# Optimization experiments

Measured on AMD Instinct MI355X. Metric: run time of the kernel, lower is better.

The kernel has to match this reference:

```python
import jax, jax.numpy as jnp
import numpy as np

B, P, NOBJ = 16, 19248, 32
NUM_CLASSES = 81  # 80 foreground + background (code uses num_classes+1 w/o focal loss)
POS_TH, NEG_TH = 0.5, 0.4
VAR0, VAR1 = 0.1, 0.2  # standard SSD encode variances
NEGPOS_RATIO = 3


def setup_inputs() -> dict:
    key = jax.random.key(0)
    k1, k2, k3, k4, k5 = jax.random.split(key, 5)
    loc_data = jax.random.normal(k1, (B, P, 4), jnp.float32)
    conf_data = jax.random.normal(k2, (B, P, NUM_CLASSES), jnp.float32)
    # priors in (cx, cy, w, h), normalized coords
    pc = jax.random.uniform(k3, (P, 2), jnp.float32, 0.05, 0.95)
    pw = jax.random.uniform(jax.random.fold_in(k3, 1), (P, 2), jnp.float32, 0.05, 0.4)
    priors = jnp.concatenate([pc, pw], -1)
    # gt boxes in point form (xmin, ymin, xmax, ymax)
    gc = jax.random.uniform(k4, (B, NOBJ, 2), jnp.float32, 0.2, 0.8)
    gw = jax.random.uniform(jax.random.fold_in(k4, 1), (B, NOBJ, 2), jnp.float32, 0.05, 0.3)
    gt_boxes = jnp.concatenate([gc - gw / 2, gc + gw / 2], -1)
    gt_labels = jax.random.randint(k5, (B, NOBJ), 0, NUM_CLASSES - 1)  # 0..79
    return {"loc_data": loc_data, "conf_data": conf_data, "priors": priors,
            "gt_boxes": gt_boxes, "gt_labels": gt_labels}


def _point_form(p):
    # (cx,cy,w,h) -> (xmin,ymin,xmax,ymax)
    return jnp.concatenate([p[..., :2] - p[..., 2:] / 2, p[..., :2] + p[..., 2:] / 2], -1)


def _jaccard(a, b):
    # a: [N,4], b: [P,4] point form -> IoU [N,P]
    lt = jnp.maximum(a[:, None, :2], b[None, :, :2])
    rb = jnp.minimum(a[:, None, 2:], b[None, :, 2:])
    wh = jnp.clip(rb - lt, 0.0)
    inter = wh[..., 0] * wh[..., 1]
    area_a = (a[:, 2] - a[:, 0]) * (a[:, 3] - a[:, 1])
    area_b = (b[:, 2] - b[:, 0]) * (b[:, 3] - b[:, 1])
    return inter / (area_a[:, None] + area_b[None, :] - inter)


def _match_one(gt, labels, priors_pf, priors):
    # SSD match: per-prior best gt + force each gt's best prior to be positive
    ov = _jaccard(gt, priors_pf)                 # [N,P]
    best_prior_idx = jnp.argmax(ov, axis=1)      # [N]
    best_truth_ov = jnp.max(ov, axis=0)          # [P]
    best_truth_idx = jnp.argmax(ov, axis=0)      # [P]
    best_truth_ov = best_truth_ov.at[best_prior_idx].set(2.0)
    best_truth_idx = best_truth_idx.at[best_prior_idx].set(jnp.arange(gt.shape[0]))
    matched = gt[best_truth_idx]                 # [P,4] point form
    conf = labels[best_truth_idx] + 1
    conf = jnp.where(best_truth_ov < POS_TH, -1, conf)   # neutral band
    conf = jnp.where(best_truth_ov < NEG_TH, 0, conf)    # background
    # encode offsets with variances
    m_cxcy = (matched[:, :2] + matched[:, 2:]) / 2
    m_wh = matched[:, 2:] - matched[:, :2]
    g_cxcy = (m_cxcy - priors[:, :2]) / (VAR0 * priors[:, 2:])
    g_wh = jnp.log(m_wh / priors[:, 2:]) / VAR1
    return jnp.concatenate([g_cxcy, g_wh], -1), conf


def reference(loc_data, conf_data, priors, gt_boxes, gt_labels):
    priors_pf = _point_form(priors)
    loc_t, conf_t = jax.vmap(lambda g, l: _match_one(g, l, priors_pf, priors))(gt_boxes, gt_labels)
    loc_t = jax.lax.stop_gradient(loc_t)
    pos = conf_t > 0                                   # [B,P]
    n_pos = pos.sum(axis=1)                            # [B]
    N = jnp.maximum(pos.sum(), 1).astype(loc_data.dtype)
    # localization: smooth L1 over positives
    d = loc_data - loc_t
    ad = jnp.abs(d)
    sl1 = jnp.where(ad < 1.0, 0.5 * d * d, ad - 0.5)
    loss_l = jnp.sum(sl1 * pos[..., None])
    # confidence: hard negative mining at 3:1
    logp = jax.nn.log_softmax(conf_data, axis=-1)      # [B,P,C]
    ct = jnp.maximum(conf_t, 0)
    nll = -jnp.take_along_axis(logp, ct[..., None], axis=-1)[..., 0]  # [B,P]
    mine = jnp.where(pos | (conf_t < 0), 0.0, nll)     # exclude pos & neutral from mining
    rank = jnp.argsort(jnp.argsort(-mine, axis=1), axis=1)
    num_neg = jnp.minimum(NEGPOS_RATIO * n_pos, P - 1)
    neg = (rank < num_neg[:, None]) & (conf_t == 0)
    loss_c = jnp.sum(nll * (pos | neg))
    return jnp.stack([loss_l, loss_c]) / N
```

## Files before the change

kernel.cpp:

```cpp
#include <hip/hip_runtime.h>
#include <cstdint>
#include <cstddef>

#define BB 16
#define PP 19248
#define NOBJ 32
#define NCLS 81
#define POS_TH 0.5f
#define NEG_TH 0.4f
#define VAR0 0.1f
#define VAR1 0.2f
#define NEGPOS 3

#define MTB 256
#define NMB ((PP + MTB - 1) / MTB)
#define MAINB 1024
#define ROWS_PB 128
#define NSLOT ((PP + ROWS_PB - 1) / ROWS_PB)
#define NSLOTW (NSLOT * 16)
#define ST 1024

#define MCH 8
#define CHLEN (PP / MCH)
#define MJOBS (BB * NOBJ * MCH)
#define MBLK (MJOBS / 4)

#define HSHIFT 19
#define HSIZE 8192
#define HPT (HSIZE / ST)
#define CAP HSIZE

__global__ __launch_bounds__(MTB) void k_match(const float* __restrict__ priors,
                                               const float* __restrict__ gt_boxes,
                                               unsigned long long* __restrict__ gkey) {
    const int wid = threadIdx.x >> 6, lane = threadIdx.x & 63;
    const int job = blockIdx.x * 4 + wid;
    const int b = job >> 8;
    const int n = (job >> 3) & 31;
    const int c = job & 7;

    const float4 g = ((const float4*)gt_boxes)[b * NOBJ + n];
    float garea;
    {
#pragma clang fp contract(off)
        garea = (g.z - g.x) * (g.w - g.y);
    }

    unsigned long long bestkey = 0ull;
    const int pbeg = c * CHLEN;
    const int pend = pbeg + CHLEN;
    for (int p = pbeg + lane; p < pend; p += 64) {
        float4 pr = ((const float4*)priors)[p];
        float iou;
        {
#pragma clang fp contract(off)
            float hw = pr.z / 2.0f, hh = pr.w / 2.0f;
            float px1 = pr.x - hw, py1 = pr.y - hh, px2 = pr.x + hw, py2 = pr.y + hh;
            float parea = (px2 - px1) * (py2 - py1);
            float ix1 = fmaxf(g.x, px1), iy1 = fmaxf(g.y, py1);
            float ix2 = fminf(g.z, px2), iy2 = fminf(g.w, py2);
            float iw = fmaxf(ix2 - ix1, 0.0f), ih = fmaxf(iy2 - iy1, 0.0f);
            float inter = iw * ih;
            iou = inter / (garea + parea - inter);
        }
        unsigned long long key = (((unsigned long long)__float_as_uint(iou)) << 32) |
                                 (unsigned long long)(0xFFFFFFFFu - (unsigned)p);
        if (key > bestkey) bestkey = key;
    }
#pragma unroll
    for (int m = 1; m < 64; m <<= 1) {
        unsigned long long o = __shfl_xor(bestkey, m, 64);
        if (o > bestkey) bestkey = o;
    }
    if (lane == 0) atomicMax(&gkey[b * NOBJ + n], bestkey);
}

__global__ __launch_bounds__(MTB) void k_prior(const float* __restrict__ priors,
                                               const float* __restrict__ gt_boxes,
                                               const int* __restrict__ gt_labels,
                                               unsigned* __restrict__ bp) {
    const int b = blockIdx.y;
    const int p = blockIdx.x * MTB + threadIdx.x;
    __shared__ float4 sg[NOBJ];
    __shared__ int slab[NOBJ];
    if (threadIdx.x < NOBJ) {
        sg[threadIdx.x] = ((const float4*)gt_boxes)[b * NOBJ + threadIdx.x];
        slab[threadIdx.x] = gt_labels[b * NOBJ + threadIdx.x];
    }
    __syncthreads();
    if (p >= PP) return;

    float4 pr = ((const float4*)priors)[p];
    float px1, py1, px2, py2, parea;
    {
#pragma clang fp contract(off)
        float hw = pr.z / 2.0f, hh = pr.w / 2.0f;
        px1 = pr.x - hw; py1 = pr.y - hh; px2 = pr.x + hw; py2 = pr.y + hh;
        parea = (px2 - px1) * (py2 - py1);
    }

    float best = -1.0f;
    int bn = 0;
#pragma unroll 4
    for (int n = 0; n < NOBJ; ++n) {
        float4 g = sg[n];
        float iou;
        {
#pragma clang fp contract(off)
            float ix1 = fmaxf(g.x, px1), iy1 = fmaxf(g.y, py1);
            float ix2 = fminf(g.z, px2), iy2 = fminf(g.w, py2);
            float iw = fmaxf(ix2 - ix1, 0.0f), ih = fmaxf(iy2 - iy1, 0.0f);
            float inter = iw * ih;
            float garea = (g.z - g.x) * (g.w - g.y);
            iou = inter / (garea + parea - inter);
        }
        if (iou > best) { best = iou; bn = n; }
    }
    unsigned cc;
    if (best < NEG_TH) cc = 1u;
    else if (best < POS_TH) cc = 0u;
    else cc = (unsigned)(slab[bn] + 2);
    bp[(size_t)b * PP + p] = ((unsigned)bn << 8) | cc;
}

__global__ __launch_bounds__(512) void k_force(const int* __restrict__ gt_labels,
                                               const unsigned long long* __restrict__ gkey,
                                               unsigned* __restrict__ bp) {
    const int i = threadIdx.x;
    const int b = i >> 5, n = i & 31;
    unsigned long long key = gkey[b * NOBJ + n];
    unsigned pstar = 0xFFFFFFFFu - (unsigned)(key & 0xFFFFFFFFull);
    int lab = gt_labels[b * NOBJ + n];
    unsigned val = 0x80000000u | ((unsigned)n << 8) | (unsigned)(lab + 2);
    atomicMax(&bp[(size_t)b * PP + pstar], val);
}

__device__ __forceinline__ float sl1(float d) {
    float ad = fabsf(d);
    return ad < 1.0f ? 0.5f * d * d : ad - 0.5f;
}

__global__ __launch_bounds__(MAINB) void k_main(const float* __restrict__ loc_data,
                                                const float* __restrict__ conf_data,
                                                const float* __restrict__ priors,
                                                const float* __restrict__ gt_boxes,
                                                const unsigned* __restrict__ bp,
                                                float* __restrict__ mine,
                                                float* __restrict__ p_ll,
                                                float* __restrict__ p_lc,
                                                int* __restrict__ p_np) {
    const int b = blockIdx.y;
    const int t = threadIdx.x;
    const int wid = t >> 6;
    const int lane = t & 63;
    const int g = lane >> 3;
    const int j = lane & 7;
    const int rbase = blockIdx.x * ROWS_PB + wid * 8;
    const int r = rbase + g;
    const bool valid = r < PP;
    const int slot = blockIdx.x * 16 + wid;

    const float* rowp = conf_data + ((size_t)b * PP + r) * NCLS;
    float c[10];
#pragma unroll
    for (int i = 0; i < 10; ++i) c[i] = 0.0f;
    float c80 = 0.0f;
    unsigned w = 1u;
    if (valid) {
#pragma unroll
        for (int i = 0; i < 10; ++i) c[i] = rowp[j + 8 * i];
        if (j == 0) c80 = rowp[80];
        w = bp[(size_t)b * PP + r];
    }

    float s = 0.0f;
#pragma unroll
    for (int i = 0; i < 10; ++i) s += __expf(c[i]);
    if (j == 0) s += __expf(c80);
    s += __shfl_xor(s, 1, 64);
    s += __shfl_xor(s, 2, 64);
    s += __shfl_xor(s, 4, 64);
    const float lse = __logf(s);

    const int cc = (int)(w & 0xFFu);

    float my_ll = 0.0f, my_lc = 0.0f;
    int my_pos = 0;

    if (valid && j == 0) {
        mine[(size_t)b * PP + r] = (cc == 1) ? (lse - c[0]) : 0.0f;
        if (cc >= 2) {
            my_pos = 1;
            my_lc = lse - rowp[cc - 1];
            const int ti = (int)((w >> 8) & 63u);
            float4 gbox = ((const float4*)gt_boxes)[b * NOBJ + ti];
            float4 pr = ((const float4*)priors)[r];
            float mcx = (gbox.x + gbox.z) / 2.0f, mcy = (gbox.y + gbox.w) / 2.0f;
            float mw = gbox.z - gbox.x, mh = gbox.w - gbox.y;
            float t0 = (mcx - pr.x) / (VAR0 * pr.z);
            float t1 = (mcy - pr.y) / (VAR0 * pr.w);
            float t2 = logf(mw / pr.z) / VAR1;
            float t3 = logf(mh / pr.w) / VAR1;
            float4 ld = ((const float4*)loc_data)[(size_t)b * PP + r];
            my_ll = sl1(ld.x - t0) + sl1(ld.y - t1) + sl1(ld.z - t2) + sl1(ld.w - t3);
        }
    }

    if (__ballot(my_pos != 0) == 0ull) {
        if (lane == 0) {
            p_ll[b * NSLOTW + slot] = 0.0f;
            p_lc[b * NSLOTW + slot] = 0.0f;
            p_np[b * NSLOTW + slot] = 0;
        }
    } else {
        for (int off = 32; off > 0; off >>= 1) {
            my_ll += __shfl_down(my_ll, off, 64);
            my_lc += __shfl_down(my_lc, off, 64);
            my_pos += __shfl_down(my_pos, off, 64);
        }
        if (lane == 0) {
            p_ll[b * NSLOTW + slot] = my_ll;
            p_lc[b * NSLOTW + slot] = my_lc;
            p_np[b * NSLOTW + slot] = my_pos;
        }
    }
}

__global__ __launch_bounds__(ST) void k_select(const float* __restrict__ mine,
                                               const float* __restrict__ p_ll,
                                               const float* __restrict__ p_lc,
                                               const int* __restrict__ p_np,
                                               float* __restrict__ acc,
                                               int* __restrict__ acc_np,
                                               unsigned* __restrict__ done,
                                               float* __restrict__ out) {
    const int b = blockIdx.x;
    const int tid = threadIdx.x;
    const int wid = tid >> 6, lane = tid & 63;
    constexpr int NW = ST / 64;

    __shared__ unsigned hist[HSIZE];
    __shared__ unsigned s_tsum[ST];
    __shared__ unsigned s_wsum[NW];
    __shared__ float rll[NW], rlc[NW];
    __shared__ int rnp[NW];
    __shared__ float rs1[NW], rs2[NW];
    __shared__ unsigned rc2[NW];
    __shared__ float s_ll, s_lc, s_neg;
    __shared__ int s_np, s_B, s_G1;
    __shared__ unsigned s_cntB, s_cnt, s_prefix;
    __shared__ int s_rem;
    __shared__ unsigned h16[16];
    __shared__ unsigned swh[NW * 16];
    __shared__ unsigned stot[16];

    float ll = 0.0f, lc = 0.0f;
    int np = 0;
    for (int i = tid; i < NSLOTW; i += ST) {
        ll += p_ll[b * NSLOTW + i];
        lc += p_lc[b * NSLOTW + i];
        np += p_np[b * NSLOTW + i];
    }
    for (int off = 32; off > 0; off >>= 1) {
        ll += __shfl_down(ll, off, 64);
        lc += __shfl_down(lc, off, 64);
        np += __shfl_down(np, off, 64);
    }
    if (lane == 0) { rll[wid] = ll; rlc[wid] = lc; rnp[wid] = np; }
    __syncthreads();
    if (tid == 0) {
        float a = 0.0f, c = 0.0f;
        int n = 0;
        for (int w = 0; w < NW; ++w) { a += rll[w]; c += rlc[w]; n += rnp[w]; }
        s_ll = a; s_lc = c; s_np = n;
        s_neg = 0.0f;
    }
    __syncthreads();
    const int np_b = s_np;
    const int k = min(NEGPOS * np_b, PP - 1);

    const float* mv = mine + (size_t)b * PP;
    const float4* mv4 = (const float4*)mv;
    constexpr int PP4 = PP / 4;

    if (k > 0) {
        for (int i = tid; i < HSIZE; i += ST) hist[i] = 0u;
        __syncthreads();
        for (int i = tid; i < PP4; i += ST) {
            float4 v = mv4[i];
            atomicAdd(&hist[__float_as_uint(v.x) >> HSHIFT], 1u);
            atomicAdd(&hist[__float_as_uint(v.y) >> HSHIFT], 1u);
            atomicAdd(&hist[__float_as_uint(v.z) >> HSHIFT], 1u);
            atomicAdd(&hist[__float_as_uint(v.w) >> HSHIFT], 1u);
        }
        __syncthreads();

        unsigned tsum = 0;
        const int hb = tid * HPT;
#pragma unroll
        for (int v = 0; v < HPT; ++v) tsum += hist[hb + v];
        s_tsum[tid] = tsum;
        unsigned wsum = tsum;
        for (int off = 32; off > 0; off >>= 1) wsum += __shfl_down(wsum, off, 64);
        if (lane == 0) s_wsum[wid] = wsum;
        __syncthreads();
        if (tid == 0) {
            unsigned cum = 0;
            int w = NW - 1;
            for (; w > 0; --w) {
                if (cum + s_wsum[w] >= (unsigned)k) break;
                cum += s_wsum[w];
            }
            int t = (w + 1) * 64 - 1;
            for (; t > w * 64; --t) {
                if (cum + s_tsum[t] >= (unsigned)k) break;
                cum += s_tsum[t];
            }
            int bin = t * HPT + HPT - 1;
            for (; bin > t * HPT; --bin) {
                if (cum + hist[bin] >= (unsigned)k) break;
                cum += hist[bin];
            }
            s_B = bin;
            s_G1 = (int)cum;
            s_cntB = hist[bin];
            s_cnt = 0u;
        }
        __syncthreads();
        const int B = s_B;
        const int r = k - s_G1;
        const unsigned cntB = s_cntB;
        const unsigned bin_lo = (unsigned)B << HSHIFT;
        const unsigned hi_base = (unsigned)(B + 1) << HSHIFT;
        unsigned* cbuf = hist;

        if (cntB <= CAP) {
            float S1 = 0.0f;
            for (int i = tid; i < PP4; i += ST) {
                float4 v = mv4[i];
                unsigned bx = __float_as_uint(v.x);
                unsigned by = __float_as_uint(v.y);
                unsigned bz = __float_as_uint(v.z);
                unsigned bw = __float_as_uint(v.w);
                if (bx >= hi_base) S1 += v.x;
                else if (bx >= bin_lo) cbuf[atomicAdd(&s_cnt, 1u)] = bx;
                if (by >= hi_base) S1 += v.y;
                else if (by >= bin_lo) cbuf[atomicAdd(&s_cnt, 1u)] = by;
                if (bz >= hi_base) S1 += v.z;
                else if (bz >= bin_lo) cbuf[atomicAdd(&s_cnt, 1u)] = bz;
                if (bw >= hi_base) S1 += v.w;
                else if (bw >= bin_lo) cbuf[atomicAdd(&s_cnt, 1u)] = bw;
            }
            for (int off = 32; off > 0; off >>= 1) S1 += __shfl_down(S1, off, 64);
            if (lane == 0) rs1[wid] = S1;
            __syncthreads();

            if (tid == 0) { s_prefix = bin_lo; s_rem = r; }
            __syncthreads();
            for (int pass = 0; pass < 5; ++pass) {
                const int shift = (pass < 4) ? (15 - 4 * pass) : 0;
                const int width = (pass < 4) ? 4 : 3;
                const int nb = 1 << width;
                const unsigned hm = 0xFFFFFFFFu << (shift + width);
                if (tid < 16) h16[tid] = 0u;
                __syncthreads();
                const unsigned prefix = s_prefix;
                for (unsigned i = tid; i < cntB; i += ST) {
                    unsigned bits = cbuf[i];
                    if ((bits & hm) == prefix)
                        atomicAdd(&h16[(bits >> shift) & (nb - 1)], 1u);
                }
                __syncthreads();
                if (tid == 0) {
                    int rem = s_rem;
                    unsigned cum = 0;
                    int chosen = 0;
                    for (int v = nb - 1; v >= 0; --v) {
                        unsigned c = h16[v];
                        if (cum + c >= (unsigned)rem) { chosen = v; s_rem = rem - (int)cum; break; }
                        cum += c;
                    }
                    s_prefix = prefix | ((unsigned)chosen << shift);
                }
                __syncthreads();
            }
            const unsigned T = s_prefix;

            float S2 = 0.0f;
            unsigned c2 = 0;
            for (unsigned i = tid; i < cntB; i += ST) {
                unsigned bits = cbuf[i];
                if (bits > T) { S2 += __uint_as_float(bits); c2++; }
            }
            for (int off = 32; off > 0; off >>= 1) {
                S2 += __shfl_down(S2, off, 64);
                c2 += __shfl_down(c2, off, 64);
            }
            if (lane == 0) { rs2[wid] = S2; rc2[wid] = c2; }
            __syncthreads();
            if (tid == 0) {
                float S1t = 0.0f, S2t = 0.0f;
                unsigned c2t = 0;
                for (int w = 0; w < NW; ++w) { S1t += rs1[w]; S2t += rs2[w]; c2t += rc2[w]; }
                s_neg = S1t + S2t + (float)(r - (int)c2t) * __uint_as_float(T);
            }
            __syncthreads();
        } else {
            if (tid == 0) { s_prefix = 0u; s_rem = k; }
            __syncthreads();
            for (int pass = 0; pass < 8; ++pass) {
                const int shift = 28 - 4 * pass;
                const unsigned hm = (pass == 0) ? 0u : (0xFFFFFFFFu << (shift + 4));
                const unsigned prefix = s_prefix;
                unsigned cnt[16];
#pragma unroll
                for (int v = 0; v < 16; ++v) cnt[v] = 0u;
                for (int i = tid; i < PP; i += ST) {
                    unsigned bits = __float_as_uint(mv[i]);
                    unsigned key = ((bits & hm) == prefix) ? ((bits >> shift) & 15u) : 16u;
                    if (__any(key != 16u)) {
#pragma unroll
                        for (int v = 0; v < 16; ++v)
                            cnt[v] += (unsigned)__popcll(__ballot(key == (unsigned)v));
                    }
                }
                if (lane == 0) {
#pragma unroll
                    for (int v = 0; v < 16; ++v) swh[wid * 16 + v] = cnt[v];
                }
                __syncthreads();
                if (tid < 16) {
                    unsigned tt = 0;
#pragma unroll
                    for (int w = 0; w < NW; ++w) tt += swh[w * 16 + tid];
                    stot[tid] = tt;
                }
                __syncthreads();
                if (tid == 0) {
                    int rem = s_rem;
                    unsigned cum = 0;
                    int chosen = 0;
                    for (int v = 15; v >= 0; --v) {
                        unsigned c = stot[v];
                        if (cum + c >= (unsigned)rem) { chosen = v; s_rem = rem - (int)cum; break; }
                        cum += c;
                    }
                    s_prefix = prefix | ((unsigned)chosen << shift);
                }
                __syncthreads();
            }
            const unsigned T = s_prefix;
            float sum = 0.0f;
            unsigned cnt = 0;
            for (int i = tid; i < PP; i += ST) {
                float v = mv[i];
                if (__float_as_uint(v) > T) { sum += v; cnt++; }
            }
            for (int off = 32; off > 0; off >>= 1) {
                sum += __shfl_down(sum, off, 64);
                cnt += __shfl_down(cnt, off, 64);
            }
            if (lane == 0) { rs2[wid] = sum; rc2[wid] = cnt; }
            __syncthreads();
            if (tid == 0) {
                float S = 0.0f;
                int G = 0;
                for (int w = 0; w < NW; ++w) { S += rs2[w]; G += (int)rc2[w]; }
                s_neg = S + (float)(k - G) * __uint_as_float(T);
            }
            __syncthreads();
        }
    }

    if (tid == 0) {
        atomicAdd(&acc[0], s_ll);
        atomicAdd(&acc[1], s_lc + s_neg);
        atomicAdd(acc_np, np_b);
        __threadfence();
        unsigned prev = atomicAdd(done, 1u);
        if (prev == BB - 1) {
            int tp = atomicAdd(acc_np, 0);
            float N = (float)max(tp, 1);
            float a0 = atomicAdd(&acc[0], 0.0f);
            float a1 = atomicAdd(&acc[1], 0.0f);
            out[0] = a0 / N;
            out[1] = a1 / N;
        }
    }
}

extern "C" void kernel_launch(void* const* d_in, const int* in_sizes, int n_in,
                              void* d_out, int out_size, void* d_ws, size_t ws_size,
                              hipStream_t stream) {
    const float* loc    = (const float*)d_in[0];
    const float* conf   = (const float*)d_in[1];
    const float* priors = (const float*)d_in[2];
    const float* gt     = (const float*)d_in[3];
    const int*   labels = (const int*)d_in[4];
    float* out = (float*)d_out;

    char* ws = (char*)d_ws;
    const size_t SZ_BP = (size_t)BB * PP * 4;
    const size_t SZ_SLOT = (size_t)BB * NSLOTW * 4;
    unsigned long long* gkey = (unsigned long long*)ws;
    float*    acc    = (float*)   (ws + 4096);
    int*      acc_np = (int*)     (ws + 4104);
    unsigned* done   = (unsigned*)(ws + 4108);
    unsigned* bp  = (unsigned*)(ws + 4224);
    float* mine = (float*)(ws + 4224 + SZ_BP);
    float* p_ll = (float*)(ws + 4224 + 2 * SZ_BP);
    float* p_lc = (float*)(ws + 4224 + 2 * SZ_BP + SZ_SLOT);
    int*   p_np = (int*)  (ws + 4224 + 2 * SZ_BP + 2 * SZ_SLOT);

    (void)hipMemsetAsync(ws, 0, 4224, stream);

    k_match<<<MBLK, MTB, 0, stream>>>(priors, gt, gkey);

    dim3 pg(NMB, BB);
    k_prior<<<pg, MTB, 0, stream>>>(priors, gt, labels, bp);

    k_force<<<1, 512, 0, stream>>>(labels, gkey, bp);

    dim3 kg(NSLOT, BB);
    k_main<<<kg, MAINB, 0, stream>>>(loc, conf, priors, gt, bp,
                                     mine, p_ll, p_lc, p_np);

    k_select<<<BB, ST, 0, stream>>>(mine, p_ll, p_lc, p_np, acc, acc_np, done, out);
}
```

Before: 210.7 us.

## Merge match and prior kernels; parallelize bin search and small-bucket select

Combines the per-gt best-prior kernel and the per-prior best-gt kernel into one launch, with block index choosing the role, so one launch and its gap are removed. In the selection kernel, the serial single-thread histogram bin search becomes a wavefront suffix-scan with ballot. When the threshold bucket holds at most 1024 elements, a direct O(n^2) rank-by-comparison replaces the five radix refinement passes and their barriers. The quadratic comparison could cost more when the bucket is near 1024 elements.

```diff
diff --git a/kernel.cpp b/kernel.cpp
--- a/kernel.cpp
+++ b/kernel.cpp
@@ -24,103 +24,105 @@
 #define CHLEN (PP / MCH)
 #define MJOBS (BB * NOBJ * MCH)
 #define MBLK (MJOBS / 4)
+#define MPBLK (MBLK + NMB * BB)
 
 #define HSHIFT 19
 #define HSIZE 8192
 #define HPT (HSIZE / ST)
 #define CAP HSIZE
 
-__global__ __launch_bounds__(MTB) void k_match(const float* __restrict__ priors,
-                                               const float* __restrict__ gt_boxes,
-                                               unsigned long long* __restrict__ gkey) {
-    const int wid = threadIdx.x >> 6, lane = threadIdx.x & 63;
-    const int job = blockIdx.x * 4 + wid;
-    const int b = job >> 8;
-    const int n = (job >> 3) & 31;
-    const int c = job & 7;
-
-    const float4 g = ((const float4*)gt_boxes)[b * NOBJ + n];
-    float garea;
-    {
+__global__ __launch_bounds__(MTB) void k_mp(const float* __restrict__ priors,
+                                            const float* __restrict__ gt_boxes,
+                                            const int* __restrict__ gt_labels,
+                                            unsigned long long* __restrict__ gkey,
+                                            unsigned* __restrict__ bp) {
+    if (blockIdx.x < MBLK) {
+        const int wid = threadIdx.x >> 6, lane = threadIdx.x & 63;
+        const int job = blockIdx.x * 4 + wid;
+        const int b = job >> 8;
+        const int n = (job >> 3) & 31;
+        const int c = job & 7;
+
+        const float4 g = ((const float4*)gt_boxes)[b * NOBJ + n];
+        float garea;
+        {
 #pragma clang fp contract(off)
-        garea = (g.z - g.x) * (g.w - g.y);
-    }
-
-    unsigned long long bestkey = 0ull;
-    const int pbeg = c * CHLEN;
-    const int pend = pbeg + CHLEN;
-    for (int p = pbeg + lane; p < pend; p += 64) {
+            garea = (g.z - g.x) * (g.w - g.y);
+        }
+
+        unsigned long long bestkey = 0ull;
+        const int pbeg = c * CHLEN;
+        const int pend = pbeg + CHLEN;
+        for (int p = pbeg + lane; p < pend; p += 64) {
+            float4 pr = ((const float4*)priors)[p];
+            float iou;
+            {
+#pragma clang fp contract(off)
+                float hw = pr.z / 2.0f, hh = pr.w / 2.0f;
+                float px1 = pr.x - hw, py1 = pr.y - hh, px2 = pr.x + hw, py2 = pr.y + hh;
+                float parea = (px2 - px1) * (py2 - py1);
+                float ix1 = fmaxf(g.x, px1), iy1 = fmaxf(g.y, py1);
+                float ix2 = fminf(g.z, px2), iy2 = fminf(g.w, py2);
+                float iw = fmaxf(ix2 - ix1, 0.0f), ih = fmaxf(iy2 - iy1, 0.0f);
+                float inter = iw * ih;
+                iou = inter / (garea + parea - inter);
+            }
+            unsigned long long key = (((unsigned long long)__float_as_uint(iou)) << 32) |
+                                     (unsigned long long)(0xFFFFFFFFu - (unsigned)p);
+            if (key > bestkey) bestkey = key;
+        }
+#pragma unroll
+        for (int m = 1; m < 64; m <<= 1) {
+            unsigned long long o = __shfl_xor(bestkey, m, 64);
+            if (o > bestkey) bestkey = o;
+        }
+        if (lane == 0) atomicMax(&gkey[b * NOBJ + n], bestkey);
+    } else {
+        const int bx = blockIdx.x - MBLK;
+        const int b = bx / NMB;
+        const int cx = bx - b * NMB;
+        const int p = cx * MTB + threadIdx.x;
+        __shared__ float4 sg[NOBJ];
+        __shared__ int slab[NOBJ];
+        if (threadIdx.x < NOBJ) {
+            sg[threadIdx.x] = ((const float4*)gt_boxes)[b * NOBJ + threadIdx.x];
+            slab[threadIdx.x] = gt_labels[b * NOBJ + threadIdx.x];
+        }
+        __syncthreads();
+        if (p >= PP) return;
+
         float4 pr = ((const float4*)priors)[p];
-        float iou;
+        float px1, py1, px2, py2, parea;
         {
 #pragma clang fp contract(off)
             float hw = pr.z / 2.0f, hh = pr.w / 2.0f;
-            float px1 = pr.x - hw, py1 = pr.y - hh, px2 = pr.x + hw, py2 = pr.y + hh;
-            float parea = (px2 - px1) * (py2 - py1);
-            float ix1 = fmaxf(g.x, px1), iy1 = fmaxf(g.y, py1);
-            float ix2 = fminf(g.z, px2), iy2 = fminf(g.w, py2);
-            float iw = fmaxf(ix2 - ix1, 0.0f), ih = fmaxf(iy2 - iy1, 0.0f);
-            float inter = iw * ih;
-            iou = inter / (garea + parea - inter);
-        }
-        unsigned long long key = (((unsigned long long)__float_as_uint(iou)) << 32) |
-                                 (unsigned long long)(0xFFFFFFFFu - (unsigned)p);
-        if (key > bestkey) bestkey = key;
-    }
-#pragma unroll
-    for (int m = 1; m < 64; m <<= 1) {
-        unsigned long long o = __shfl_xor(bestkey, m, 64);
-        if (o > bestkey) bestkey = o;
-    }
-    if (lane == 0) atomicMax(&gkey[b * NOBJ + n], bestkey);
-}
-
-__global__ __launch_bounds__(MTB) void k_prior(const float* __restrict__ priors,
-                                               const float* __restrict__ gt_boxes,
-                                               const int* __restrict__ gt_labels,
-                                               unsigned* __restrict__ bp) {
-    const int b = blockIdx.y;
-    const int p = blockIdx.x * MTB + threadIdx.x;
-    __shared__ float4 sg[NOBJ];
-    __shared__ int slab[NOBJ];
-    if (threadIdx.x < NOBJ) {
-        sg[threadIdx.x] = ((const float4*)gt_boxes)[b * NOBJ + threadIdx.x];
-        slab[threadIdx.x] = gt_labels[b * NOBJ + threadIdx.x];
-    }
-    __syncthreads();
-    if (p >= PP) return;
-
-    float4 pr = ((const float4*)priors)[p];
-    float px1, py1, px2, py2, parea;
-    {
+            px1 = pr.x - hw; py1 = pr.y - hh; px2 = pr.x + hw; py2 = pr.y + hh;
+            parea = (px2 - px1) * (py2 - py1);
+        }
+
+        float best = -1.0f;
+        int bn = 0;
+#pragma unroll 4
+        for (int n = 0; n < NOBJ; ++n) {
+            float4 g = sg[n];
+            float iou;
+            {
 #pragma clang fp contract(off)
-        float hw = pr.z / 2.0f, hh = pr.w / 2.0f;
-        px1 = pr.x - hw; py1 = pr.y - hh; px2 = pr.x + hw; py2 = pr.y + hh;
-        parea = (px2 - px1) * (py2 - py1);
-    }
-
-    float best = -1.0f;
-    int bn = 0;
-#pragma unroll 4
-    for (int n = 0; n < NOBJ; ++n) {
-        float4 g = sg[n];
-        float iou;
-        {
-#pragma clang fp contract(off)
-            float ix1 = fmaxf(g.x, px1), iy1 = fmaxf(g.y, py1);
-            float ix2 = fminf(g.z, px2), iy2 = fminf(g.w, py2);
-            float iw = fmaxf(ix2 - ix1, 0.0f), ih = fmaxf(iy2 - iy1, 0.0f);
-            float inter = iw * ih;
-            float garea = (g.z - g.x) * (g.w - g.y);
-            iou = inter / (garea + parea - inter);
-        }
-        if (iou > best) { best = iou; bn = n; }
-    }
-    unsigned cc;
-    if (best < NEG_TH) cc = 1u;
-    else if (best < POS_TH) cc = 0u;
-    else cc = (unsigned)(slab[bn] + 2);
-    bp[(size_t)b * PP + p] = ((unsigned)bn << 8) | cc;
+                float ix1 = fmaxf(g.x, px1), iy1 = fmaxf(g.y, py1);
+                float ix2 = fminf(g.z, px2), iy2 = fminf(g.w, py2);
+                float iw = fmaxf(ix2 - ix1, 0.0f), ih = fmaxf(iy2 - iy1, 0.0f);
+                float inter = iw * ih;
+                float garea = (g.z - g.x) * (g.w - g.y);
+                iou = inter / (garea + parea - inter);
+            }
+            if (iou > best) { best = iou; bn = n; }
+        }
+        unsigned cc;
+        if (best < NEG_TH) cc = 1u;
+        else if (best < POS_TH) cc = 0u;
+        else cc = (unsigned)(slab[bn] + 2);
+        bp[(size_t)b * PP + p] = ((unsigned)bn << 8) | cc;
+    }
 }
 
 __global__ __launch_bounds__(512) void k_force(const int* __restrict__ gt_labels,
@@ -304,27 +306,45 @@
         for (int off = 32; off > 0; off >>= 1) wsum += __shfl_down(wsum, off, 64);
         if (lane == 0) s_wsum[wid] = wsum;
         __syncthreads();
-        if (tid == 0) {
-            unsigned cum = 0;
-            int w = NW - 1;
-            for (; w > 0; --w) {
-                if (cum + s_wsum[w] >= (unsigned)k) break;
-                cum += s_wsum[w];
-            }
-            int t = (w + 1) * 64 - 1;
-            for (; t > w * 64; --t) {
-                if (cum + s_tsum[t] >= (unsigned)k) break;
-                cum += s_tsum[t];
-            }
-            int bin = t * HPT + HPT - 1;
-            for (; bin > t * HPT; --bin) {
-                if (cum + hist[bin] >= (unsigned)k) break;
-                cum += hist[bin];
-            }
-            s_B = bin;
-            s_G1 = (int)cum;
-            s_cntB = hist[bin];
-            s_cnt = 0u;
+        if (wid == 0) {
+            unsigned x1 = (lane < NW) ? s_wsum[lane] : 0u;
+            unsigned suf1 = x1;
+#pragma unroll
+            for (int off = 1; off < 64; off <<= 1) {
+                unsigned y = __shfl_down(suf1, off, 64);
+                if (lane + off < 64) suf1 += y;
+            }
+            unsigned long long m1 = __ballot((lane < NW) && (suf1 >= (unsigned)k));
+            const int wstar = 63 - __builtin_clzll(m1);
+            const unsigned a1 = __shfl(suf1, wstar, 64) - __shfl(x1, wstar, 64);
+            unsigned x2 = s_tsum[wstar * 64 + lane];
+            unsigned suf2 = x2;
+#pragma unroll
+            for (int off = 1; off < 64; off <<= 1) {
+                unsigned y = __shfl_down(suf2, off, 64);
+                if (lane + off < 64) suf2 += y;
+            }
+            unsigned long long m2 = __ballot(a1 + suf2 >= (unsigned)k);
+            const int lstar = 63 - __builtin_clzll(m2);
+            const unsigned a2 = a1 + __shfl(suf2, lstar, 64) - __shfl(x2, lstar, 64);
+            const int hb0 = (wstar * 64 + lstar) * HPT;
+            unsigned x3 = (lane < HPT) ? hist[hb0 + lane] : 0u;
+            unsigned suf3 = x3;
+#pragma unroll
+            for (int off = 1; off < 8; off <<= 1) {
+                unsigned y = __shfl_down(suf3, off, 64);
+                if (lane + off < 8) suf3 += y;
+            }
+            unsigned long long m3 = __ballot((lane < HPT) && (a2 + suf3 >= (unsigned)k));
+            const int vstar = 63 - __builtin_clzll(m3);
+            const unsigned g1v = a2 + __shfl(suf3, vstar, 64) - __shfl(x3, vstar, 64);
+            const unsigned cb = __shfl(x3, vstar, 64);
+            if (lane == 0) {
+                s_B = hb0 + vstar;
+                s_G1 = (int)g1v;
+                s_cntB = cb;
+                s_cnt = 0u;
+            }
         }
         __syncthreads();
         const int B = s_B;
@@ -355,34 +375,48 @@
             if (lane == 0) rs1[wid] = S1;
             __syncthreads();
 
-            if (tid == 0) { s_prefix = bin_lo; s_rem = r; }
-            __syncthreads();
-            for (int pass = 0; pass < 5; ++pass) {
-                const int shift = (pass < 4) ? (15 - 4 * pass) : 0;
-                const int width = (pass < 4) ? 4 : 3;
-                const int nb = 1 << width;
-                const unsigned hm = 0xFFFFFFFFu << (shift + width);
-                if (tid < 16) h16[tid] = 0u;
-                __syncthreads();
-                const unsigned prefix = s_prefix;
-                for (unsigned i = tid; i < cntB; i += ST) {
-                    unsigned bits = cbuf[i];
-                    if ((bits & hm) == prefix)
-                        atomicAdd(&h16[(bits >> shift) & (nb - 1)], 1u);
+            if (cntB <= 1024u) {
+                if (tid < (int)cntB) {
+                    unsigned bi = cbuf[tid];
+                    unsigned gcnt = 0, ecnt = 0;
+                    for (unsigned q = 0; q < cntB; ++q) {
+                        unsigned bq = cbuf[q];
+                        gcnt += (bq > bi) ? 1u : 0u;
+                        ecnt += (bq == bi) ? 1u : 0u;
+                    }
+                    if ((int)gcnt < r && r <= (int)(gcnt + ecnt)) s_prefix = bi;
                 }
                 __syncthreads();
-                if (tid == 0) {
-                    int rem = s_rem;
-                    unsigned cum = 0;
-                    int chosen = 0;
-                    for (int v = nb - 1; v >= 0; --v) {
-                        unsigned c = h16[v];
-                        if (cum + c >= (unsigned)rem) { chosen = v; s_rem = rem - (int)cum; break; }
-                        cum += c;
+            } else {
+                if (tid == 0) { s_prefix = bin_lo; s_rem = r; }
+                __syncthreads();
+                for (int pass = 0; pass < 5; ++pass) {
+                    const int shift = (pass < 4) ? (15 - 4 * pass) : 0;
+                    const int width = (pass < 4) ? 4 : 3;
+                    const int nb = 1 << width;
+                    const unsigned hm = 0xFFFFFFFFu << (shift + width);
+                    if (tid < 16) h16[tid] = 0u;
+                    __syncthreads();
+                    const unsigned prefix = s_prefix;
+                    for (unsigned i = tid; i < cntB; i += ST) {
+                        unsigned bits = cbuf[i];
+                        if ((bits & hm) == prefix)
+                            atomicAdd(&h16[(bits >> shift) & (nb - 1)], 1u);
                     }
-                    s_prefix = prefix | ((unsigned)chosen << shift);
+                    __syncthreads();
+                    if (tid == 0) {
+                        int rem = s_rem;
+                        unsigned cum = 0;
+                        int chosen = 0;
+                        for (int v = nb - 1; v >= 0; --v) {
+                            unsigned c = h16[v];
+                            if (cum + c >= (unsigned)rem) { chosen = v; s_rem = rem - (int)cum; break; }
+                            cum += c;
+                        }
+                        s_prefix = prefix | ((unsigned)chosen << shift);
+                    }
+                    __syncthreads();
                 }
-                __syncthreads();
             }
             const unsigned T = s_prefix;
 
@@ -514,10 +548,7 @@
 
     (void)hipMemsetAsync(ws, 0, 4224, stream);
 
-    k_match<<<MBLK, MTB, 0, stream>>>(priors, gt, gkey);
-
-    dim3 pg(NMB, BB);
-    k_prior<<<pg, MTB, 0, stream>>>(priors, gt, labels, bp);
+    k_mp<<<MPBLK, MTB, 0, stream>>>(priors, gt, labels, gkey, bp);
 
     k_force<<<1, 512, 0, stream>>>(labels, gkey, bp);
 
```

Measured after the change: 222.0 us. 5.3% more time.
